# Kernel optimization log

Measured on AMD Instinct MI355X. Metric: run time of the kernel, lower is better.

The kernel has to match this reference:

```python
import jax, jax.numpy as jnp
import numpy as np

B, T, C = 4, 2048, 2048
H, N = 32, 64  # heads, head_size
EPS = 1e-5


def setup_inputs() -> dict:
    key = jax.random.key(0)
    ks = jax.random.split(key, 16)
    s = 0.02
    return {
        'hidden': jax.random.normal(ks[0], (B, T, C), jnp.float32),
        'time_decay': jax.random.normal(ks[1], (H, N), jnp.float32),
        'time_first': jax.random.normal(ks[2], (H, N), jnp.float32),
        'Wr': jax.random.normal(ks[3], (C, C), jnp.float32) * s,
        'Wk': jax.random.normal(ks[4], (C, C), jnp.float32) * s,
        'Wv': jax.random.normal(ks[5], (C, C), jnp.float32) * s,
        'Wg': jax.random.normal(ks[6], (C, C), jnp.float32) * s,
        'Wo': jax.random.normal(ks[7], (C, C), jnp.float32) * s,
        'mix_r': jax.random.uniform(ks[8], (1, 1, C), jnp.float32),
        'mix_k': jax.random.uniform(ks[9], (1, 1, C), jnp.float32),
        'mix_v': jax.random.uniform(ks[10], (1, 1, C), jnp.float32),
        'mix_g': jax.random.uniform(ks[11], (1, 1, C), jnp.float32),
        'ln_w': jax.random.uniform(ks[12], (C,), jnp.float32, 0.5, 1.5),
        'ln_b': jax.random.normal(ks[13], (C,), jnp.float32) * 0.1,
        'init_state': jnp.zeros((B, H, N, N), jnp.float32),
    }


def reference(hidden, time_decay, time_first, Wr, Wk, Wv, Wg, Wo,
              mix_r, mix_k, mix_v, mix_g, ln_w, ln_b, init_state):
    b, t, c = hidden.shape
    h, n = time_decay.shape
    # time shift: shifted[:, 0] = 0 (fresh state), shifted[:, i] = hidden[:, i-1]
    shifted = jnp.pad(hidden, ((0, 0), (1, 0), (0, 0)))[:, :-1]
    xk = hidden * mix_k + shifted * (1.0 - mix_k)
    xv = hidden * mix_v + shifted * (1.0 - mix_v)
    xr = hidden * mix_r + shifted * (1.0 - mix_r)
    xg = hidden * mix_g + shifted * (1.0 - mix_g)

    r = (xr @ Wr).astype(jnp.float32).reshape(b, t, h, n)
    k = (xk @ Wk).astype(jnp.float32).reshape(b, t, h, n)
    v = (xv @ Wv).astype(jnp.float32).reshape(b, t, h, n)
    gate = jax.nn.silu(xg @ Wg)  # [b,t,c]

    w = jnp.exp(-jnp.exp(time_decay.astype(jnp.float32)))  # [h,n] decay per k-channel
    u = time_first.astype(jnp.float32)                      # [h,n]

    def step(state, rkv):
        rt, kt, vt = rkv  # each [b,h,n]
        at = kt[..., :, None] * vt[..., None, :]  # outer product kt @ vt -> [b,h,n,n]
        out_t = jnp.einsum('bhn,bhnm->bhm', rt, u[None, :, :, None] * at + state)
        new_state = at + w[None, :, :, None] * state
        return new_state, out_t

    rT = jnp.moveaxis(r, 1, 0)  # [t,b,h,n]
    kT = jnp.moveaxis(k, 1, 0)
    vT = jnp.moveaxis(v, 1, 0)
    final_state, outT = jax.lax.scan(step, init_state.astype(jnp.float32), (rT, kT, vT))
    out = jnp.moveaxis(outT, 0, 1)  # [b,t,h,n]

    # GroupNorm with num_groups = h over the c = h*n channels
    mean = out.mean(-1, keepdims=True)
    var = out.var(-1, keepdims=True)
    out = (out - mean) / jnp.sqrt(var + EPS)
    out = out.reshape(b, t, c) * ln_w + ln_b

    out = out.astype(hidden.dtype) * gate
    out = out @ Wo
    return out, final_state
```

## Files before the change

### kernel.cpp

```cpp
#include <hip/hip_runtime.h>
#include <stdint.h>

typedef unsigned short ushort_t;
typedef __attribute__((ext_vector_type(8))) short bf16x8;
typedef __attribute__((ext_vector_type(4))) float f32x4;
typedef __attribute__((ext_vector_type(8))) unsigned short u16x8;

__device__ __forceinline__ ushort_t f2bf(float f) {
  union { float f; unsigned u; } v; v.f = f;
  unsigned r = v.u + 0x7fffu + ((v.u >> 16) & 1u);
  return (ushort_t)(r >> 16);
}
__device__ __forceinline__ float bf2f(ushort_t u) {
  union { unsigned u; float f; } v; v.u = ((unsigned)u) << 16;
  return v.f;
}

__device__ __forceinline__ void gload_lds16(const void* g, void* l) {
  __builtin_amdgcn_global_load_lds(
      (const __attribute__((address_space(1))) void*)g,
      (__attribute__((address_space(3))) void*)l, 16, 0, 0);
}

struct PrepArgs {
  const float* W[5];
  ushort_t* Wt[5];
  const float* Hd;
  const float* mr; const float* mk; const float* mv; const float* mg;
  ushort_t* xr; ushort_t* xk; ushort_t* xv; ushort_t* xg;
};

__global__ __launch_bounds__(256) void prep(PrepArgs a, int n, int Mrows, int Tt) {
  const int z = blockIdx.z;
  if (z < 5) {
    const float* __restrict__ W = a.W[z];
    ushort_t* __restrict__ Wt = a.Wt[z];
    __shared__ float tile[32][33];
    const int tx = threadIdx.x & 31, ty = threadIdx.x >> 5;
    const int bx = blockIdx.x, by = blockIdx.y;
#pragma unroll
    for (int r = 0; r < 4; ++r)
      tile[ty + 8 * r][tx] = W[(size_t)(by * 32 + ty + 8 * r) * n + bx * 32 + tx];
    __syncthreads();
#pragma unroll
    for (int r = 0; r < 4; ++r)
      Wt[(size_t)(bx * 32 + ty + 8 * r) * n + by * 32 + tx] =
          f2bf(tile[tx][ty + 8 * r]);
    return;
  }
  const int Cc = n;
  const float* __restrict__ Hd = a.Hd;
  const size_t n8 = (size_t)Mrows * Cc / 8;
  const int bid = blockIdx.y * gridDim.x + blockIdx.x;
  for (size_t idx = (size_t)bid * blockDim.x + threadIdx.x; idx < n8;
       idx += (size_t)gridDim.x * gridDim.y * blockDim.x) {
    const size_t e = idx * 8;
    const int m = (int)(e / (size_t)Cc);
    const int c = (int)(e % (size_t)Cc);
    const int t = m % Tt;
    f32x4 h0 = *(const f32x4*)&Hd[e];
    f32x4 h1 = *(const f32x4*)&Hd[e + 4];
    f32x4 sA = {0.f, 0.f, 0.f, 0.f}, sB = {0.f, 0.f, 0.f, 0.f};
    if (t != 0) {
      sA = *(const f32x4*)&Hd[e - Cc];
      sB = *(const f32x4*)&Hd[e - Cc + 4];
    }
    f32x4 mA[4], mB[4];
    mA[0] = *(const f32x4*)&a.mr[c]; mB[0] = *(const f32x4*)&a.mr[c + 4];
    mA[1] = *(const f32x4*)&a.mk[c]; mB[1] = *(const f32x4*)&a.mk[c + 4];
    mA[2] = *(const f32x4*)&a.mv[c]; mB[2] = *(const f32x4*)&a.mv[c + 4];
    mA[3] = *(const f32x4*)&a.mg[c]; mB[3] = *(const f32x4*)&a.mg[c + 4];
    u16x8 o[4];
#pragma unroll
    for (int w = 0; w < 4; ++w) {
#pragma unroll
      for (int q = 0; q < 4; ++q) {
        o[w][q]     = f2bf(sA[q] + (h0[q] - sA[q]) * mA[w][q]);
        o[w][q + 4] = f2bf(sB[q] + (h1[q] - sB[q]) * mB[w][q]);
      }
    }
    *(u16x8*)&a.xr[e] = o[0];
    *(u16x8*)&a.xk[e] = o[1];
    *(u16x8*)&a.xv[e] = o[2];
    *(u16x8*)&a.xg[e] = o[3];
  }
}

struct GemmArgs {
  const ushort_t* A[4];
  const ushort_t* Bt[4];
  void* C[4];
};

__device__ __forceinline__ void stage_mat(const ushort_t* __restrict__ base,
                                          int K, int voff, char* ldsmat,
                                          int tid) {
#pragma unroll
  for (int hf = 0; hf < 2; ++hf)
#pragma unroll
    for (int s = 0; s < 2; ++s)
      gload_lds16(base + (size_t)(hf * 128 + s * 64) * K + voff,
                  ldsmat + hf * 16384 + s * 8192 + tid * 16);
}

template <int BF16OUT>
__global__ __launch_bounds__(512, 1) void gemm256(GemmArgs args, int M, int N, int K) {
  extern __shared__ char lds[];
  const int z = blockIdx.z;
  const ushort_t* __restrict__ A = args.A[z];
  const ushort_t* __restrict__ Bt = args.Bt[z];

  const int tid = threadIdx.x;
  const int lane = tid & 63, w = tid >> 6;
  const int wm = w >> 2, wn = w & 3;
  const int r16 = lane & 15, kb = lane >> 4;

  const int nbx = N >> 8;
  const int nwg = nbx * (M >> 8);
  const int orig = blockIdx.y * nbx + blockIdx.x;
  const int wid = (orig & 7) * (nwg >> 3) + (orig >> 3);
  const int bm0 = (wid / nbx) << 8;
  const int bn0 = (wid % nbx) << 8;

  const int trow = tid >> 3;
  const int voff = trow * K + (((((tid & 7) * 16) ^ ((trow & 7) << 4))) >> 1);
  const ushort_t* __restrict__ Abase = A + (size_t)bm0 * K;
  const ushort_t* __restrict__ Bbase = Bt + (size_t)bn0 * K;

  int aoff[8], boff[4];
#pragma unroll
  for (int mi = 0; mi < 8; ++mi) {
    const int d = (mi * 16 + r16) * 128 + kb * 16;
    aoff[mi] = wm * 16384 + (d ^ (((d >> 7) & 7) << 4));
  }
#pragma unroll
  for (int ni = 0; ni < 4; ++ni) {
    const int d = ((wn & 1) * 64 + ni * 16 + r16) * 128 + kb * 16;
    boff[ni] = 32768 + (wn >> 1) * 16384 + (d ^ (((d >> 7) & 7) << 4));
  }

  f32x4 acc[8][4] = {};
  const int NT = K >> 6;

  stage_mat(Abase, K, voff, lds, tid);
  stage_mat(Bbase, K, voff, lds + 32768, tid);
  stage_mat(Abase + 64, K, voff, lds + 65536, tid);
  stage_mat(Bbase + 64, K, voff, lds + 65536 + 32768, tid);
  asm volatile("s_waitcnt vmcnt(8)" ::: "memory");
  asm volatile("s_barrier" ::: "memory");

  for (int t = 0; t < NT; ++t) {
    const int cur = t & 1;
    char* cbase = lds + cur * 65536;
    bf16x8 ah[4][2], bq[4][2];

#pragma unroll
    for (int m = 0; m < 4; ++m) {
      ah[m][0] = *(const bf16x8*)(cbase + aoff[m]);
      ah[m][1] = *(const bf16x8*)(cbase + (aoff[m] ^ 64));
    }
#pragma unroll
    for (int n = 0; n < 2; ++n) {
      bq[n][0] = *(const bf16x8*)(cbase + boff[n]);
      bq[n][1] = *(const bf16x8*)(cbase + (boff[n] ^ 64));
    }
    asm volatile("s_barrier" ::: "memory");
    __builtin_amdgcn_s_setprio(1);
#pragma unroll
    for (int m = 0; m < 4; ++m)
#pragma unroll
      for (int n = 0; n < 2; ++n)
#pragma unroll
        for (int ks = 0; ks < 2; ++ks)
          acc[m][n] = __builtin_amdgcn_mfma_f32_16x16x32_bf16(
              ah[m][ks], bq[n][ks], acc[m][n], 0, 0, 0);
    __builtin_amdgcn_s_setprio(0);

#pragma unroll
    for (int n = 2; n < 4; ++n) {
      bq[n][0] = *(const bf16x8*)(cbase + boff[n]);
      bq[n][1] = *(const bf16x8*)(cbase + (boff[n] ^ 64));
    }
    asm volatile("s_barrier" ::: "memory");
    __builtin_amdgcn_s_setprio(1);
#pragma unroll
    for (int m = 0; m < 4; ++m)
#pragma unroll
      for (int n = 2; n < 4; ++n)
#pragma unroll
        for (int ks = 0; ks < 2; ++ks)
          acc[m][n] = __builtin_amdgcn_mfma_f32_16x16x32_bf16(
              ah[m][ks], bq[n][ks], acc[m][n], 0, 0, 0);
    __builtin_amdgcn_s_setprio(0);

#pragma unroll
    for (int m = 0; m < 4; ++m) {
      ah[m][0] = *(const bf16x8*)(cbase + aoff[4 + m]);
      ah[m][1] = *(const bf16x8*)(cbase + (aoff[4 + m] ^ 64));
    }
    asm volatile("s_barrier" ::: "memory");
    if (t + 2 < NT)
      stage_mat(Abase + (t + 2) * 64, K, voff, cbase, tid);
    __builtin_amdgcn_s_setprio(1);
#pragma unroll
    for (int m = 0; m < 4; ++m)
#pragma unroll
      for (int n = 0; n < 2; ++n)
#pragma unroll
        for (int ks = 0; ks < 2; ++ks)
          acc[4 + m][n] = __builtin_amdgcn_mfma_f32_16x16x32_bf16(
              ah[m][ks], bq[n][ks], acc[4 + m][n], 0, 0, 0);

    if (t + 2 < NT)
      stage_mat(Bbase + (t + 2) * 64, K, voff, cbase + 32768, tid);
#pragma unroll
    for (int m = 0; m < 4; ++m)
#pragma unroll
      for (int n = 2; n < 4; ++n)
#pragma unroll
        for (int ks = 0; ks < 2; ++ks)
          acc[4 + m][n] = __builtin_amdgcn_mfma_f32_16x16x32_bf16(
              ah[m][ks], bq[n][ks], acc[4 + m][n], 0, 0, 0);
    __builtin_amdgcn_s_setprio(0);

    if (t + 1 < NT) {
      if (t + 2 < NT)
        asm volatile("s_waitcnt vmcnt(8)" ::: "memory");
      else
        asm volatile("s_waitcnt vmcnt(0)" ::: "memory");
      asm volatile("s_barrier" ::: "memory");
    }
  }

  const int row0 = bm0 + wm * 128 + kb * 4;
  const int col0 = bn0 + wn * 64 + r16;
#pragma unroll
  for (int mi = 0; mi < 8; ++mi)
#pragma unroll
    for (int ni = 0; ni < 4; ++ni) {
      f32x4 v = acc[mi][ni];
      const int row = row0 + mi * 16;
      const int col = col0 + ni * 16;
#pragma unroll
      for (int rr = 0; rr < 4; ++rr) {
        if (BF16OUT)
          ((ushort_t*)args.C[z])[(size_t)(row + rr) * N + col] = f2bf(v[rr]);
        else
          ((float*)args.C[z])[(size_t)(row + rr) * N + col] = v[rr];
      }
    }
}

__global__ __launch_bounds__(512, 1) void wkv_chunk(
    const ushort_t* __restrict__ Rm, const ushort_t* __restrict__ Km,
    const ushort_t* __restrict__ Vm, const float* __restrict__ td,
    const float* __restrict__ tf,
    float* __restrict__ Oatt, float* __restrict__ chunkA,
    int Tt, int Hh, int NC, int Lc) {
  extern __shared__ char smem[];
  ushort_t* Rs  = (ushort_t*)(smem + 0);
  ushort_t* Ks  = (ushort_t*)(smem + 18432);
  ushort_t* Ks2 = (ushort_t*)(smem + 36864);
  ushort_t* Vt  = (ushort_t*)(smem + 55296);
  ushort_t* Kt  = (ushort_t*)(smem + 72704);
  ushort_t* At  = (ushort_t*)(smem + 90112);
  float* wp   = (float*)(smem + 124928);
  float* w16p = (float*)(smem + 129280);
  float* u_   = (float*)(smem + 131456);

  const int blk = blockIdx.x;
  const int bh = blk / NC, c = blk % NC;
  const int b = bh / Hh, h = bh % Hh;
  const int tid = threadIdx.x;
  const int lane = tid & 63, w = tid >> 6;
  const int r16 = lane & 15, g = lane >> 4;
  const int Cc = Hh * 64;
  const size_t base = ((size_t)b * Tt + (size_t)c * Lc) * Cc + h * 64;

  const int srow = tid >> 2;
  const int scol = (tid & 3) * 16;
  const size_t gb = base + (size_t)srow * Cc + scol;
  u16x8 r0 = *(const u16x8*)&Rm[gb];
  u16x8 r1 = *(const u16x8*)&Rm[gb + 8];
  u16x8 k0 = *(const u16x8*)&Km[gb];
  u16x8 k1 = *(const u16x8*)&Km[gb + 8];
  u16x8 v0 = *(const u16x8*)&Vm[gb];
  u16x8 v1 = *(const u16x8*)&Vm[gb + 8];

  if (tid < 64) {
    const float ev = expf(td[h * 64 + tid]);
    const float wv = expf(-ev);
    u_[tid] = tf[h * 64 + tid];
    float p = 1.f;
#pragma unroll
    for (int d = 0; d < 16; ++d) { wp[d * 68 + tid] = p; p *= wv; }
    float pq = 1.f;
#pragma unroll
    for (int q = 0; q < 8; ++q) { w16p[q * 68 + tid] = pq; pq *= p; }
  }
  __syncthreads();

  {
    *(u16x8*)&Rs[srow * 72 + scol] = r0;
    *(u16x8*)&Rs[srow * 72 + scol + 8] = r1;
    *(u16x8*)&Ks[srow * 72 + scol] = k0;
    *(u16x8*)&Ks[srow * 72 + scol + 8] = k1;
    const int s16 = srow & 15, shi = srow >> 4;
    const float* fa = &wp[(15 - s16) * 68 + scol];
    const float* gq = &w16p[(7 - shi) * 68 + scol];
    u16x8 a2, b2;
#pragma unroll
    for (int e = 0; e < 8; ++e) {
      a2[e] = f2bf(bf2f(k0[e]) * fa[e]);
      b2[e] = f2bf(bf2f(k1[e]) * fa[e + 8]);
    }
    *(u16x8*)&Ks2[srow * 72 + scol] = a2;
    *(u16x8*)&Ks2[srow * 72 + scol + 8] = b2;
#pragma unroll
    for (int e = 0; e < 8; ++e) {
      Vt[(scol + e) * 136 + srow] = v0[e];
      Vt[(scol + 8 + e) * 136 + srow] = v1[e];
      Kt[(scol + e) * 136 + srow] = f2bf(bf2f(k0[e]) * fa[e] * gq[e]);
      Kt[(scol + 8 + e) * 136 + srow] =
          f2bf(bf2f(k1[e]) * fa[e + 8] * gq[e + 8]);
    }
    const u16x8 z = {};
    for (int o = tid; o < (128 * 136) / 8; o += 512) *(u16x8*)&At[o * 8] = z;
  }
  __syncthreads();

  for (int p = w; p < 28; p += 8) {
    int tau = 1, cum = 0;
    while (cum + tau <= p) { cum += tau; ++tau; }
    const int sig = p - cum;
    const float* wr  = &wp[r16 * 68];
    const float* w16 = &w16p[(tau - sig - 1) * 68];
    f32x4 acc = {0.f, 0.f, 0.f, 0.f};
#pragma unroll
    for (int ks = 0; ks < 2; ++ks) {
      const int ib = ks * 32 + g * 8;
      u16x8 rv = *(const u16x8*)&Rs[(tau * 16 + r16) * 72 + ib];
      bf16x8 kv = *(const bf16x8*)&Ks2[(sig * 16 + r16) * 72 + ib];
      f32x4 wa = *(const f32x4*)&wr[ib];
      f32x4 wb = *(const f32x4*)&wr[ib + 4];
      f32x4 sa = *(const f32x4*)&w16[ib];
      f32x4 sb = *(const f32x4*)&w16[ib + 4];
      union { bf16x8 v; ushort_t s[8]; } af;
#pragma unroll
      for (int e = 0; e < 4; ++e) {
        af.s[e]     = f2bf(bf2f(rv[e]) * (wa[e] * sa[e]));
        af.s[e + 4] = f2bf(bf2f(rv[e + 4]) * (wb[e] * sb[e]));
      }
      acc = __builtin_amdgcn_mfma_f32_16x16x32_bf16(af.v, kv, acc, 0, 0, 0);
    }
#pragma unroll
    for (int r = 0; r < 4; ++r)
      At[(tau * 16 + g * 4 + r) * 136 + sig * 16 + r16] = f2bf(acc[r]);
  }

  for (int rr = 0; rr < 3; ++rr) {
    const int eid = tid + rr * 512;
    if (eid >= 1088) break;
    const int tile = eid / 136;
    const int e2 = eid % 136;
    int t = 0, cum = 0;
    while (cum + t + 1 <= e2) { cum += t + 1; ++t; }
    const int s = e2 - cum;
    const ushort_t* rrow = &Rs[(tile * 16 + t) * 72];
    const ushort_t* krow = &Ks[(tile * 16 + s) * 72];
    const float* frow = (s < t) ? &wp[(t - s - 1) * 68] : u_;
    float acc = 0.f;
#pragma unroll
    for (int i0 = 0; i0 < 64; i0 += 8) {
      u16x8 rv = *(const u16x8*)&rrow[i0];
      u16x8 kv = *(const u16x8*)&krow[i0];
      f32x4 f0 = *(const f32x4*)&frow[i0];
      f32x4 f1 = *(const f32x4*)&frow[i0 + 4];
#pragma unroll
      for (int e = 0; e < 4; ++e) {
        acc = fmaf(bf2f(rv[e]), bf2f(kv[e]) * f0[e], acc);
        acc = fmaf(bf2f(rv[e + 4]), bf2f(kv[e + 4]) * f1[e], acc);
      }
    }
    At[(tile * 16 + t) * 136 + tile * 16 + s] = f2bf(acc);
  }
  __syncthreads();

  {
    const int nk = (w + 2) >> 1;
#pragma unroll
    for (int jt = 0; jt < 4; ++jt) {
      f32x4 acc = {0.f, 0.f, 0.f, 0.f};
      for (int kk = 0; kk < nk; ++kk) {
        bf16x8 af = *(const bf16x8*)&At[(w * 16 + r16) * 136 + kk * 32 + g * 8];
        bf16x8 bv = *(const bf16x8*)&Vt[(jt * 16 + r16) * 136 + kk * 32 + g * 8];
        acc = __builtin_amdgcn_mfma_f32_16x16x32_bf16(af, bv, acc, 0, 0, 0);
      }
#pragma unroll
      for (int r = 0; r < 4; ++r)
        Oatt[base + (size_t)(w * 16 + g * 4 + r) * Cc + jt * 16 + r16] = acc[r];
    }
  }

#pragma unroll
  for (int q = 0; q < 2; ++q) {
    const int T = w * 2 + q;
    const int it = T >> 2, jt = T & 3;
    f32x4 acc = {0.f, 0.f, 0.f, 0.f};
#pragma unroll
    for (int kk = 0; kk < 4; ++kk) {
      const int s0 = kk * 32 + g * 8;
      bf16x8 af = *(const bf16x8*)&Kt[(it * 16 + r16) * 136 + s0];
      bf16x8 bv = *(const bf16x8*)&Vt[(jt * 16 + r16) * 136 + s0];
      acc = __builtin_amdgcn_mfma_f32_16x16x32_bf16(af, bv, acc, 0, 0, 0);
    }
#pragma unroll
    for (int r = 0; r < 4; ++r)
      chunkA[(size_t)blk * 4096 + (it * 16 + g * 4 + r) * 64 + jt * 16 + r16] =
          acc[r];
  }
}

__global__ __launch_bounds__(256) void chunk_carry(
    const float* __restrict__ chunkA, const float* __restrict__ s0,
    const float* __restrict__ td,
    float* __restrict__ chunkS, float* __restrict__ Sout,
    int Hh, int NC, int Lc) {
  const int blk = blockIdx.x;
  const int bh = blk >> 2, q = blk & 3;
  const int h = bh % Hh;
  const int e4 = q * 1024 + threadIdx.x * 4;
  const int i = e4 >> 6;
  const float wL = expf(-(float)Lc * expf(td[h * 64 + i]));
  f32x4 S = *(const f32x4*)&s0[(size_t)bh * 4096 + e4];
  for (int c = 0; c < NC; ++c) {
    *(f32x4*)&chunkS[((size_t)bh * NC + c) * 4096 + e4] = S;
    f32x4 A = *(const f32x4*)&chunkA[((size_t)bh * NC + c) * 4096 + e4];
#pragma unroll
    for (int t = 0; t < 4; ++t) S[t] = fmaf(wL, S[t], A[t]);
  }
  *(f32x4*)&Sout[(size_t)bh * 4096 + e4] = S;
}

__global__ __launch_bounds__(512) void chunk_out(
    const float* __restrict__ OattIn, const float* __restrict__ chunkS,
    const ushort_t* __restrict__ Rm, const ushort_t* __restrict__ Gm,
    const float* __restrict__ td,
    const float* __restrict__ lnw, const float* __restrict__ lnb,
    ushort_t* __restrict__ Xo, int Tt, int Hh, int NC, int Lc) {
  __shared__ ushort_t rLb[128 * 72];
  __shared__ ushort_t St[64 * 72];
  __shared__ float Ob[128 * 68];
  __shared__ float wp[16 * 68];
  __shared__ float w16p[8 * 68];

  const int blk = blockIdx.x;
  const int bh = blk / NC, c = blk % NC;
  const int b = bh / Hh, h = bh % Hh;
  const int tid = threadIdx.x;
  const int lane = tid & 63, w = tid >> 6;
  const int r16 = lane & 15, g = lane >> 4;
  const int Cc = Hh * 64;
  const size_t rowbase = (size_t)b * Tt + (size_t)c * Lc;

  const int srow = tid >> 2;
  const int scol = (tid & 3) * 16;
  u16x8 r0 = *(const u16x8*)&Rm[(rowbase + srow) * Cc + h * 64 + scol];
  u16x8 r1 = *(const u16x8*)&Rm[(rowbase + srow) * Cc + h * 64 + scol + 8];
  const int jj = tid & 63, i0 = (tid >> 6) * 8;
  float sv[8];
#pragma unroll
  for (int e = 0; e < 8; ++e)
    sv[e] = chunkS[(size_t)blk * 4096 + (i0 + e) * 64 + jj];

  if (tid < 64) {
    const float ev = expf(td[h * 64 + tid]);
    const float wv = expf(-ev);
    float p = 1.f;
#pragma unroll
    for (int d = 0; d < 16; ++d) { wp[d * 68 + tid] = p; p *= wv; }
    float pq = 1.f;
#pragma unroll
    for (int q = 0; q < 8; ++q) { w16p[q * 68 + tid] = pq; pq *= p; }
  }
  __syncthreads();

  {
    const float* fa = &wp[(srow & 15) * 68 + scol];
    const float* gq = &w16p[(srow >> 4) * 68 + scol];
    u16x8 a2, b2;
#pragma unroll
    for (int e = 0; e < 8; ++e) {
      a2[e] = f2bf(bf2f(r0[e]) * (fa[e] * gq[e]));
      b2[e] = f2bf(bf2f(r1[e]) * (fa[e + 8] * gq[e + 8]));
    }
    *(u16x8*)&rLb[srow * 72 + scol] = a2;
    *(u16x8*)&rLb[srow * 72 + scol + 8] = b2;
#pragma unroll
    for (int e = 0; e < 8; ++e) St[jj * 72 + i0 + e] = f2bf(sv[e]);
  }
  __syncthreads();

#pragma unroll
  for (int jt = 0; jt < 4; ++jt) {
    f32x4 acc;
    const int row0 = w * 16 + g * 4;
#pragma unroll
    for (int r = 0; r < 4; ++r)
      acc[r] = OattIn[(rowbase + row0 + r) * Cc + h * 64 + jt * 16 + r16];
#pragma unroll
    for (int ks = 0; ks < 2; ++ks) {
      bf16x8 af = *(const bf16x8*)&rLb[(w * 16 + r16) * 72 + ks * 32 + g * 8];
      bf16x8 bv = *(const bf16x8*)&St[(jt * 16 + r16) * 72 + ks * 32 + g * 8];
      acc = __builtin_amdgcn_mfma_f32_16x16x32_bf16(af, bv, acc, 0, 0, 0);
    }
#pragma unroll
    for (int r = 0; r < 4; ++r)
      Ob[(row0 + r) * 68 + jt * 16 + r16] = acc[r];
  }
  __syncthreads();

  const float lw = lnw[h * 64 + lane];
  const float lb = lnb[h * 64 + lane];
  for (int k = 0; k < 16; ++k) {
    const int tau = w + 8 * k;
    const size_t goff = (rowbase + tau) * Cc + h * 64 + lane;
    const float acc = Ob[tau * 68 + lane];
    float s = acc, s2 = acc * acc;
#pragma unroll
    for (int m = 1; m < 64; m <<= 1) {
      s += __shfl_xor(s, m);
      s2 += __shfl_xor(s2, m);
    }
    const float mean = s * (1.f / 64.f);
    const float var = s2 * (1.f / 64.f) - mean * mean;
    const float inv = 1.f / sqrtf(var + 1e-5f);
    const float y = (acc - mean) * inv * lw + lb;
    const float gv = bf2f(Gm[goff]);
    const float gate = gv / (1.f + expf(-gv));
    Xo[goff] = f2bf(y * gate);
  }
}

extern "C" void kernel_launch(void* const* d_in, const int* in_sizes, int n_in,
                              void* d_out, int out_size, void* d_ws, size_t ws_size,
                              hipStream_t stream) {
  const int B = 4, T = 2048, Cc = 2048, H = 32;
  const int M = B * T;
  const int NC = 16, Lc = 128;

  const float* hidden = (const float*)d_in[0];
  const float* td     = (const float*)d_in[1];
  const float* tf     = (const float*)d_in[2];
  const float* Wr     = (const float*)d_in[3];
  const float* Wk     = (const float*)d_in[4];
  const float* Wv     = (const float*)d_in[5];
  const float* Wg     = (const float*)d_in[6];
  const float* Wo     = (const float*)d_in[7];
  const float* mix_r  = (const float*)d_in[8];
  const float* mix_k  = (const float*)d_in[9];
  const float* mix_v  = (const float*)d_in[10];
  const float* mix_g  = (const float*)d_in[11];
  const float* lnw    = (const float*)d_in[12];
  const float* lnb    = (const float*)d_in[13];
  const float* s0     = (const float*)d_in[14];

  const size_t SZ_WT = (size_t)Cc * Cc * 2;
  const size_t SZ_X  = (size_t)M * Cc * 2;
  const size_t NEED  = 5 * SZ_WT + 6 * SZ_X;

  if (ws_size < NEED) return;

  float* out  = (float*)d_out;
  float* sfin = (float*)d_out + (size_t)M * Cc;
  ushort_t* xg = (ushort_t*)d_out;
  ushort_t* gb = (ushort_t*)d_out + (size_t)M * Cc;

  char* ws = (char*)d_ws;
  ushort_t* wt[5];
  for (int z = 0; z < 5; ++z) wt[z] = (ushort_t*)(ws + z * SZ_WT);
  char* regX = ws + 5 * SZ_WT;
  char* regY = regX + 3 * SZ_X;
  ushort_t* xr = (ushort_t*)regX;
  ushort_t* xk = (ushort_t*)(regX + SZ_X);
  ushort_t* xv = (ushort_t*)(regX + 2 * SZ_X);
  ushort_t* rb = (ushort_t*)regY;
  ushort_t* kb = (ushort_t*)(regY + SZ_X);
  ushort_t* vb = (ushort_t*)(regY + 2 * SZ_X);
  float* oatt   = (float*)regX;
  float* chunkA = (float*)(regX + 2 * SZ_X);
  float* chunkS = (float*)(regY + SZ_X);
  ushort_t* xo  = (ushort_t*)(regY + 2 * SZ_X);

  {
    PrepArgs a;
    a.W[0] = Wr; a.W[1] = Wk; a.W[2] = Wv; a.W[3] = Wg; a.W[4] = Wo;
    for (int z = 0; z < 5; ++z) a.Wt[z] = wt[z];
    a.Hd = hidden;
    a.mr = mix_r; a.mk = mix_k; a.mv = mix_v; a.mg = mix_g;
    a.xr = xr; a.xk = xk; a.xv = xv; a.xg = xg;
    dim3 g(Cc / 32, Cc / 32, 6);
    prep<<<g, 256, 0, stream>>>(a, Cc, M, T);
  }

  {
    const ushort_t* As[4] = {xr, xk, xv, xg};
    void* Cs[4] = {rb, kb, vb, gb};
    for (int z = 0; z < 4; ++z) {
      GemmArgs a = {};
      a.A[0] = As[z]; a.Bt[0] = wt[z]; a.C[0] = Cs[z];
      dim3 g(Cc / 256, M / 256, 1);
      gemm256<1><<<g, 512, 131072, stream>>>(a, M, Cc, Cc);
    }
  }

  wkv_chunk<<<B * H * NC, 512, 131712, stream>>>(rb, kb, vb, td, tf, oatt,
                                                 chunkA, T, H, NC, Lc);
  chunk_carry<<<B * H * 4, 256, 0, stream>>>(chunkA, s0, td, chunkS, sfin,
                                             H, NC, Lc);
  chunk_out<<<B * H * NC, 512, 0, stream>>>(oatt, chunkS, rb, gb, td, lnw, lnb,
                                            xo, T, H, NC, Lc);

  {
    GemmArgs a = {};
    a.A[0] = xo; a.Bt[0] = wt[4]; a.C[0] = out;
    dim3 g(Cc / 256, M / 256, 1);
    gemm256<0><<<g, 512, 131072, stream>>>(a, M, Cc, Cc);
  }
}
```

Measured before the change: 545.2 us.

## Swizzle transposed V/K LDS layout and balance causal intra-chunk work across warps

Transposed V and K tiles in LDS now use an XOR swizzle on the column index keyed by the 16-column group, to cut bank conflicts on the scattered transposed stores. All readers of those tiles apply the matching XOR. The attention-times-V stage is also split so each warp handles row tile w for two column tiles and row tile 7-w for the other two. This evens out the triangular causal workload that previously grew with the warp index. The XOR keeps reads within 8-element granules, but if any consumer misses the swizzle the results will be wrong.

Result: no change. 538.9 us (-1.2%).

```diff
diff --git a/kernel.cpp b/kernel.cpp
--- a/kernel.cpp
+++ b/kernel.cpp
@@ -316,12 +316,15 @@
     }
     *(u16x8*)&Ks2[srow * 72 + scol] = a2;
     *(u16x8*)&Ks2[srow * 72 + scol + 8] = b2;
+    const int key0 = ((scol >> 4) & 3) << 4;
+    const int key1 = (((scol + 8) >> 4) & 3) << 4;
+    const int sc0 = srow ^ key0, sc1 = srow ^ key1;
 #pragma unroll
     for (int e = 0; e < 8; ++e) {
-      Vt[(scol + e) * 136 + srow] = v0[e];
-      Vt[(scol + 8 + e) * 136 + srow] = v1[e];
-      Kt[(scol + e) * 136 + srow] = f2bf(bf2f(k0[e]) * fa[e] * gq[e]);
-      Kt[(scol + 8 + e) * 136 + srow] =
+      Vt[(scol + e) * 136 + sc0] = v0[e];
+      Vt[(scol + 8 + e) * 136 + sc1] = v1[e];
+      Kt[(scol + e) * 136 + sc0] = f2bf(bf2f(k0[e]) * fa[e] * gq[e]);
+      Kt[(scol + 8 + e) * 136 + sc1] =
           f2bf(bf2f(k1[e]) * fa[e + 8] * gq[e + 8]);
     }
     const u16x8 z = {};
@@ -386,19 +389,25 @@
   }
   __syncthreads();
 
-  {
-    const int nk = (w + 2) >> 1;
-#pragma unroll
-    for (int jt = 0; jt < 4; ++jt) {
+#pragma unroll
+  for (int half = 0; half < 2; ++half) {
+    const int tt = half ? (7 - w) : w;
+    const int nk = (tt + 2) >> 1;
+#pragma unroll
+    for (int j2 = 0; j2 < 2; ++j2) {
+      const int jt = half * 2 + j2;
+      const int vk = jt << 4;
       f32x4 acc = {0.f, 0.f, 0.f, 0.f};
       for (int kk = 0; kk < nk; ++kk) {
-        bf16x8 af = *(const bf16x8*)&At[(w * 16 + r16) * 136 + kk * 32 + g * 8];
-        bf16x8 bv = *(const bf16x8*)&Vt[(jt * 16 + r16) * 136 + kk * 32 + g * 8];
+        bf16x8 af = *(const bf16x8*)&At[(tt * 16 + r16) * 136 + kk * 32 + g * 8];
+        bf16x8 bv = *(const bf16x8*)&Vt[(jt * 16 + r16) * 136 +
+                                        ((kk * 32 + g * 8) ^ vk)];
         acc = __builtin_amdgcn_mfma_f32_16x16x32_bf16(af, bv, acc, 0, 0, 0);
       }
 #pragma unroll
       for (int r = 0; r < 4; ++r)
-        Oatt[base + (size_t)(w * 16 + g * 4 + r) * Cc + jt * 16 + r16] = acc[r];
+        Oatt[base + (size_t)(tt * 16 + g * 4 + r) * Cc + jt * 16 + r16] =
+            acc[r];
     }
   }
 
@@ -406,12 +415,14 @@
   for (int q = 0; q < 2; ++q) {
     const int T = w * 2 + q;
     const int it = T >> 2, jt = T & 3;
+    const int kk2 = (it & 3) << 4;
+    const int vk = jt << 4;
     f32x4 acc = {0.f, 0.f, 0.f, 0.f};
 #pragma unroll
     for (int kk = 0; kk < 4; ++kk) {
       const int s0 = kk * 32 + g * 8;
-      bf16x8 af = *(const bf16x8*)&Kt[(it * 16 + r16) * 136 + s0];
-      bf16x8 bv = *(const bf16x8*)&Vt[(jt * 16 + r16) * 136 + s0];
+      bf16x8 af = *(const bf16x8*)&Kt[(it * 16 + r16) * 136 + (s0 ^ kk2)];
+      bf16x8 bv = *(const bf16x8*)&Vt[(jt * 16 + r16) * 136 + (s0 ^ vk)];
       acc = __builtin_amdgcn_mfma_f32_16x16x32_bf16(af, bv, acc, 0, 0, 0);
     }
 #pragma unroll
```
